# Optimization experiments

Measured on AMD Instinct MI355X. Metric: run time of the kernel, lower is better.

Reference implementation:

```python
import jax, jax.numpy as jnp
import numpy as np

NPG = 128      # nodes per graph = g(4) * e(32), forced by rearrange + cnn1 channels
G, E32 = 4, 32
ALPHA = 1.0    # GCN2Conv(in_channels, 1) -> alpha = 1
BETA = 1.0     # theta=None -> beta = 1


def _gcn_norm(edge_index, edge_weight, n):
    """PyG gcn_norm: add self-loops (w=1), sym-normalize by degree at dst."""
    src, dst = edge_index[0], edge_index[1]
    loop = jnp.arange(n)
    src = jnp.concatenate([src, loop])
    dst = jnp.concatenate([dst, loop])
    w = jnp.concatenate([edge_weight, jnp.ones((n,), edge_weight.dtype)])
    deg = jax.ops.segment_sum(w, dst, num_segments=n)
    dinv = jnp.where(deg > 0, jax.lax.rsqrt(deg), 0.0)
    norm = dinv[src] * w * dinv[dst]
    return src, dst, norm


def _propagate(x, src, dst, norm, n):
    # gather -> weight -> scatter-add (SpMM)
    return jax.ops.segment_sum(x[src] * norm[:, None], dst, num_segments=n)


def setup_inputs() -> dict:
    key = jax.random.key(0)
    ks = jax.random.split(key, 10)
    N, E, C, H, CH = 65536, 524288, 128, 512, 256
    x = jax.random.normal(ks[0], (N, C), jnp.float32)
    edge_index = jax.random.randint(ks[1], (2, E), 0, N, dtype=jnp.int64)
    edge_attr = jax.random.uniform(ks[2], (E,), jnp.float32)
    w1_gcn2 = jax.random.normal(ks[3], (C, C), jnp.float32) / np.float32(np.sqrt(C))
    w_gcn = jax.random.normal(ks[4], (C, H), jnp.float32) / np.float32(np.sqrt(C))
    b_gcn = jnp.zeros((H,), jnp.float32)
    w_cnn1 = jax.random.normal(ks[5], (H, 4 * H), jnp.float32) / np.float32(np.sqrt(4 * H))
    b_cnn1 = jnp.zeros((H,), jnp.float32)
    w_cnn2 = jax.random.normal(ks[6], (CH, H), jnp.float32) / np.float32(np.sqrt(H))
    b_cnn2 = jnp.zeros((CH,), jnp.float32)
    w_lin = jax.random.normal(ks[7], (32 * CH,), jnp.float32) / np.float32(np.sqrt(32 * CH))
    b_lin = jnp.zeros((), jnp.float32)
    return {"x": x, "edge_attr": edge_attr, "w1_gcn2": w1_gcn2, "w_gcn": w_gcn,
            "b_gcn": b_gcn, "w_cnn1": w_cnn1, "b_cnn1": b_cnn1, "w_cnn2": w_cnn2,
            "b_cnn2": b_cnn2, "w_lin": w_lin, "b_lin": b_lin, "edge_index": edge_index}


def reference(x, edge_attr, w1_gcn2, w_gcn, b_gcn, w_cnn1, b_cnn1, w_cnn2, b_cnn2,
              w_lin, b_lin, edge_index):
    n = x.shape[0]
    bs = n // NPG
    src, dst, norm = _gcn_norm(edge_index, edge_attr, n)

    # GCN2Conv(C, layer=1): h = (1-a)*A_hat x + a*x0; out = (1-b)*h + b*(h @ W1)
    h = _propagate(x, src, dst, norm, n)
    h = h * (1.0 - ALPHA) + ALPHA * x
    h = (1.0 - BETA) * h + BETA * (h @ w1_gcn2)

    # GCNConv(C, H): A_hat (h @ W) + b
    h = _propagate(h @ w_gcn, src, dst, norm, n) + b_gcn
    h = jnp.tanh(h)

    f = h.shape[1]  # hidden_channels
    # '(bs g e) f -> bs (g f) e', e=32, g=4
    h = h.reshape(bs, G, E32, f).transpose(0, 1, 3, 2).reshape(bs, G * f, E32)
    # 1x1 convs == per-position linears over channel dim
    h = jax.nn.relu(jnp.einsum('bce,oc->boe', h, w_cnn1) + b_cnn1[None, :, None])
    h = jax.nn.relu(jnp.einsum('bce,oc->boe', h, w_cnn2) + b_cnn2[None, :, None])
    # dropout p=0.5 is identity in eval mode
    h = h.reshape(bs, -1)
    out = h @ w_lin + b_lin
    return jax.nn.sigmoid(out)
```

## Files before the change

### kernel.cpp

```cpp
#include <hip/hip_runtime.h>
#include <hip/hip_bf16.h>

#define N_NODES 65536
#define N_EDGES 524288

typedef __attribute__((ext_vector_type(8))) short bf16x8;
typedef __attribute__((ext_vector_type(4))) float f32x4;

__device__ __forceinline__ float bf2f(unsigned short u) {
    union { unsigned int i; float f; } v;
    v.i = ((unsigned int)u) << 16;
    return v.f;
}
__device__ __forceinline__ unsigned short f2bf(float f) {
    union { float f; unsigned int i; } v;
    v.f = f;
    unsigned int r = v.i + 0x7fff + ((v.i >> 16) & 1);
    return (unsigned short)(r >> 16);
}

__global__ void init_k(int* __restrict__ cnt, float* __restrict__ logits) {
    int i = blockIdx.x * 256 + threadIdx.x;
    cnt[i] = 0;
    if (i < 512) logits[i] = 0.0f;
}
__global__ void cnt_k(const int* __restrict__ dst, int* __restrict__ cnt) {
    int e = blockIdx.x * 256 + threadIdx.x;
    atomicAdd(&cnt[dst[e]], 1);
}

__global__ __launch_bounds__(256) void scan1_k(const int* __restrict__ cnt,
                                               int* __restrict__ rp,
                                               int* __restrict__ bsum) {
    __shared__ int s[256];
    int t = threadIdx.x, g = blockIdx.x * 256 + t;
    int v = cnt[g];
    s[t] = v;
    __syncthreads();
    for (int d = 1; d < 256; d <<= 1) {
        int u = (t >= d) ? s[t - d] : 0;
        __syncthreads();
        s[t] += u;
        __syncthreads();
    }
    rp[g] = s[t] - v;
    if (t == 255) bsum[blockIdx.x] = s[255];
}
__global__ __launch_bounds__(256) void scan2_k(int* __restrict__ bsum,
                                               int* __restrict__ rp) {
    __shared__ int s[256];
    int t = threadIdx.x;
    int v = bsum[t];
    s[t] = v;
    __syncthreads();
    for (int d = 1; d < 256; d <<= 1) {
        int u = (t >= d) ? s[t - d] : 0;
        __syncthreads();
        s[t] += u;
        __syncthreads();
    }
    bsum[t] = s[t] - v;
    if (t == 255) rp[65536] = s[255];
}
__global__ __launch_bounds__(256) void scan3_k(int* __restrict__ rp,
                                               const int* __restrict__ bsum,
                                               int* __restrict__ cursor) {
    int t = threadIdx.x, g = blockIdx.x * 256 + t;
    int r = rp[g] + bsum[blockIdx.x];
    rp[g] = r;
    cursor[g] = r;
}

__global__ void scatter_k(const int* __restrict__ src, const int* __restrict__ dst,
                          const float* __restrict__ w,
                          int* __restrict__ cursor, uint2* __restrict__ ep) {
    int e = blockIdx.x * 256 + threadIdx.x;
    int pos = atomicAdd(&cursor[dst[e]], 1);
    uint2 p;
    p.x = (unsigned int)src[e];
    p.y = __float_as_uint(w[e]);
    ep[pos] = p;
}

__global__ void rowsum_k(const int* __restrict__ rp, const uint2* __restrict__ ep,
                         float* __restrict__ dinv) {
    int n = blockIdx.x * 256 + threadIdx.x;
    int beg = rp[n], end = rp[n + 1];
    float s = 1.0f;
    for (int i = beg; i < end; ++i) s += __uint_as_float(ep[i].y);
    dinv[n] = rsqrtf(s);
}

__global__ void xscale_k(const float* __restrict__ x, const float* __restrict__ dinv,
                         __hip_bfloat16* __restrict__ xbf) {
    int i = (blockIdx.x * 256 + threadIdx.x) * 4;
    float d = dinv[i >> 7];
    float4 v = *(const float4*)(x + i);
    alignas(8) __hip_bfloat16 tmp[4] = {
        __float2bfloat16(d * v.x), __float2bfloat16(d * v.y),
        __float2bfloat16(d * v.z), __float2bfloat16(d * v.w)};
    *(ushort4*)((unsigned short*)xbf + i) = *(const ushort4*)tmp;
}

__global__ void wprep_k(const float* __restrict__ wc1, __hip_bfloat16* __restrict__ wc1pk,
                        const float* __restrict__ wc2, __hip_bfloat16* __restrict__ wc2bf,
                        const float* __restrict__ w1, const float* __restrict__ wg,
                        __hip_bfloat16* __restrict__ WTpk) {
    int bid = blockIdx.x;
    if (bid < 512) {
        int t = bid * 256 + threadIdx.x;
        int l = t & 63, grp = t >> 6;
        int kt = grp & 63, nb = grp >> 6;
        int n = nb * 16 + (l & 15);
        int k0 = kt * 32 + (l >> 4) * 8;
        const float* src = wc1 + (size_t)n * 2048 + k0;
        alignas(16) __hip_bfloat16 tmp[8];
#pragma unroll
        for (int e = 0; e < 8; ++e) tmp[e] = __float2bfloat16(src[e]);
        *(ushort4*)((unsigned short*)wc1pk + (size_t)t * 8)     = *(const ushort4*)tmp;
        *(ushort4*)((unsigned short*)wc1pk + (size_t)t * 8 + 4) = *(const ushort4*)(tmp + 4);
    } else if (bid < 640) {
        int i = (bid - 512) * 1024 + threadIdx.x * 4;
        float4 v = *(const float4*)(wc2 + i);
        alignas(8) __hip_bfloat16 tmp[4] = {__float2bfloat16(v.x), __float2bfloat16(v.y),
                                            __float2bfloat16(v.z), __float2bfloat16(v.w)};
        *(ushort4*)((unsigned short*)wc2bf + i) = *(const ushort4*)tmp;
    } else {
        int t = (bid - 640) * 256 + threadIdx.x;
        int f = t >> 7, c = t & 127;
        float s = 0.f;
#pragma unroll 8
        for (int m = 0; m < 128; ++m) s += w1[c * 128 + m] * wg[m * 512 + f];
        int pk = ((((f >> 4) * 4 + (c >> 5)) * 64 + ((c >> 3) & 3) * 16 + (f & 15)) * 8) + (c & 7);
        WTpk[pk] = __float2bfloat16(s);
    }
}

__global__ __launch_bounds__(256) void gather_k(const int* __restrict__ rp,
                                                const uint2* __restrict__ ep,
                                                const unsigned short* __restrict__ xbf,
                                                const float* __restrict__ dinv,
                                                __hip_bfloat16* __restrict__ ybf) {
    int n = (blockIdx.x * 256 + threadIdx.x) >> 6;
    int lane = threadIdx.x & 63;
    int beg = rp[n], end = rp[n + 1];
    float accx, accy;
    {
        unsigned int u = *(const unsigned int*)(xbf + (size_t)n * 128 + lane * 2);
        accx = bf2f((unsigned short)(u & 0xffff));
        accy = bf2f((unsigned short)(u >> 16));
    }
    int i = beg;
    for (; i + 8 <= end; i += 8) {
        uint2 p[8];
        unsigned int u[8];
#pragma unroll
        for (int k = 0; k < 8; ++k) p[k] = ep[i + k];
#pragma unroll
        for (int k = 0; k < 8; ++k)
            u[k] = *(const unsigned int*)(xbf + (size_t)p[k].x * 128 + lane * 2);
#pragma unroll
        for (int k = 0; k < 8; ++k) {
            float c = __uint_as_float(p[k].y);
            accx += c * bf2f((unsigned short)(u[k] & 0xffff));
            accy += c * bf2f((unsigned short)(u[k] >> 16));
        }
    }
    for (; i + 4 <= end; i += 4) {
        uint2 p[4];
        unsigned int u[4];
#pragma unroll
        for (int k = 0; k < 4; ++k) p[k] = ep[i + k];
#pragma unroll
        for (int k = 0; k < 4; ++k)
            u[k] = *(const unsigned int*)(xbf + (size_t)p[k].x * 128 + lane * 2);
#pragma unroll
        for (int k = 0; k < 4; ++k) {
            float c = __uint_as_float(p[k].y);
            accx += c * bf2f((unsigned short)(u[k] & 0xffff));
            accy += c * bf2f((unsigned short)(u[k] >> 16));
        }
    }
    for (; i < end; ++i) {
        uint2 p = ep[i];
        unsigned int u = *(const unsigned int*)(xbf + (size_t)p.x * 128 + lane * 2);
        float c = __uint_as_float(p.y);
        accx += c * bf2f((unsigned short)(u & 0xffff));
        accy += c * bf2f((unsigned short)(u >> 16));
    }
    float dn = dinv[n];
    accx *= dn;
    accy *= dn;
    alignas(4) __hip_bfloat16 o[2] = {__float2bfloat16(accx), __float2bfloat16(accy)};
    *(unsigned int*)((unsigned short*)ybf + (size_t)n * 128 + lane * 2) =
        *(const unsigned int*)o;
}

__device__ __forceinline__ void gll16(const void* g, void* l) {
    __builtin_amdgcn_global_load_lds(
        (const __attribute__((address_space(1))) void*)g,
        (__attribute__((address_space(3))) void*)l, 16, 0, 0);
}

__global__ __launch_bounds__(512) void fh2c1_k(
    const __hip_bfloat16* __restrict__ ybf,
    const __hip_bfloat16* __restrict__ WTpk,
    const float* __restrict__ bg,
    const __hip_bfloat16* __restrict__ wc1pk,
    const float* __restrict__ bc1,
    __hip_bfloat16* __restrict__ act1) {
    __shared__ char yt[8192];
    __shared__ char ht[16384];
    const int tid = threadIdx.x;
    const int lane = tid & 63, wid = tid >> 6;
    const int bx = blockIdx.x;
    const int l15 = lane & 15, lhi = lane >> 4;

    const __hip_bfloat16* Bp[4];
#pragma unroll
    for (int j = 0; j < 4; ++j)
        Bp[j] = wc1pk + ((size_t)(wid * 4 + j) * 64) * 512 + lane * 8;

    f32x4 acc[2][4] = {};

    for (int g = 0; g < 4; ++g) {
        __syncthreads();
        {
            int r = wid * 4 + (lane >> 4);
            int node = bx * 128 + g * 32 + r;
            int scol = ((lane & 15) ^ (r & 7)) << 4;
            gll16((const char*)ybf + (size_t)node * 256 + scol,
                  yt + wid * 1024 + lane * 16);
        }
        __syncthreads();

        for (int h = 0; h < 2; ++h) {
            f32x4 hacc[2][2];
#pragma unroll
            for (int i = 0; i < 2; ++i)
#pragma unroll
                for (int j = 0; j < 2; ++j) hacc[i][j] = (f32x4){0.f, 0.f, 0.f, 0.f};
#pragma unroll
            for (int kt = 0; kt < 4; ++kt) {
                bf16x8 af[2], bfr[2];
#pragma unroll
                for (int i = 0; i < 2; ++i) {
                    int r = i * 16 + l15;
                    int s = (kt * 4 + lhi) ^ (r & 7);
                    af[i] = *(const bf16x8*)(yt + r * 256 + s * 16);
                }
#pragma unroll
                for (int j = 0; j < 2; ++j) {
                    int nb = h * 16 + wid * 2 + j;
                    bfr[j] = *(const bf16x8*)(WTpk +
                        ((size_t)(nb * 4 + kt) * 64 + lane) * 8);
                }
#pragma unroll
                for (int i = 0; i < 2; ++i)
#pragma unroll
                    for (int j = 0; j < 2; ++j)
                        hacc[i][j] = __builtin_amdgcn_mfma_f32_16x16x32_bf16(
                            bfr[j], af[i], hacc[i][j], 0, 0, 0);
            }
            __syncthreads();
#pragma unroll
            for (int j = 0; j < 2; ++j) {
                int coln = h * 256 + wid * 32 + j * 16 + lhi * 4;
                float4 bgv = *(const float4*)(bg + coln);
                int bytecol = (wid * 32 + j * 16 + lhi * 4) * 2;
                int s = bytecol >> 4;
                int off8 = bytecol & 15;
#pragma unroll
                for (int i = 0; i < 2; ++i) {
                    int row = i * 16 + l15;
                    alignas(8) unsigned short o[4];
#pragma unroll
                    for (int r = 0; r < 4; ++r) {
                        float v = hacc[i][j][r] + ((const float*)&bgv)[r];
                        v = 1.0f - 2.0f / (__expf(2.0f * v) + 1.0f);
                        o[r] = f2bf(v);
                    }
                    *(uint2*)(ht + row * 512 + ((s ^ (row & 7)) << 4) + off8) =
                        *(const uint2*)o;
                }
            }
            __syncthreads();

            const int ktb = g * 16 + h * 8;
            bf16x8 b0[4], b1[4];
#pragma unroll
            for (int j = 0; j < 4; ++j)
                b0[j] = *(const bf16x8*)(Bp[j] + (size_t)ktb * 512);
#pragma unroll
            for (int kk = 0; kk < 8; kk += 2) {
#pragma unroll
                for (int j = 0; j < 4; ++j)
                    b1[j] = *(const bf16x8*)(Bp[j] + (size_t)(ktb + kk + 1) * 512);
                {
                    bf16x8 af[2];
#pragma unroll
                    for (int i = 0; i < 2; ++i) {
                        int r = i * 16 + l15;
                        int s = (kk * 4 + lhi) ^ (r & 7);
                        af[i] = *(const bf16x8*)(ht + r * 512 + s * 16);
                    }
#pragma unroll
                    for (int i = 0; i < 2; ++i)
#pragma unroll
                        for (int j = 0; j < 4; ++j)
                            acc[i][j] = __builtin_amdgcn_mfma_f32_16x16x32_bf16(
                                b0[j], af[i], acc[i][j], 0, 0, 0);
                }
                if (kk + 2 < 8) {
#pragma unroll
                    for (int j = 0; j < 4; ++j)
                        b0[j] = *(const bf16x8*)(Bp[j] + (size_t)(ktb + kk + 2) * 512);
                }
                {
                    bf16x8 af[2];
#pragma unroll
                    for (int i = 0; i < 2; ++i) {
                        int r = i * 16 + l15;
                        int s = ((kk + 1) * 4 + lhi) ^ (r & 7);
                        af[i] = *(const bf16x8*)(ht + r * 512 + s * 16);
                    }
#pragma unroll
                    for (int i = 0; i < 2; ++i)
#pragma unroll
                        for (int j = 0; j < 4; ++j)
                            acc[i][j] = __builtin_amdgcn_mfma_f32_16x16x32_bf16(
                                b1[j], af[i], acc[i][j], 0, 0, 0);
                }
            }
        }
    }

#pragma unroll
    for (int i = 0; i < 2; ++i) {
        int m = bx * 32 + i * 16 + l15;
#pragma unroll
        for (int j = 0; j < 4; ++j) {
            int n = wid * 64 + j * 16 + lhi * 4;
            float4 bv = *(const float4*)(bc1 + n);
            ushort4 o;
#pragma unroll
            for (int r = 0; r < 4; ++r) {
                float v = fmaxf(acc[i][j][r] + ((const float*)&bv)[r], 0.f);
                ((unsigned short*)&o)[r] = f2bf(v);
            }
            *(ushort4*)((unsigned short*)act1 + (size_t)m * 512 + n) = o;
        }
    }
}

template <int ACT, int OUT_MODE, int SWIZ_NTX>
__global__ __launch_bounds__(256) void gemm_mfma_k(
    const __hip_bfloat16* __restrict__ A, const __hip_bfloat16* __restrict__ B,
    const float* __restrict__ bias, void* __restrict__ Cout,
    const float* __restrict__ wlin, int M, int N, int K) {
    __shared__ char lds[65536];

    const int tid = threadIdx.x;
    const int lane = tid & 63, wid = tid >> 6;
    int bx, by;
    if (SWIZ_NTX > 0) {
        int orig = blockIdx.x;
        int per = gridDim.x / (8 * SWIZ_NTX);
        int xcd = orig & 7, k = orig >> 3;
        by = xcd * per + k / SWIZ_NTX;
        bx = k % SWIZ_NTX;
    } else {
        bx = blockIdx.x;
        by = blockIdx.y;
    }
    const int bm = by * 128, bn = bx * 128;
    const int wr = wid >> 1, wc = wid & 1;

    const int srow = wid * 16 + (lane >> 2);
    const int skcol = (((lane & 3) ^ ((lane >> 3) & 3))) * 8;
    const __hip_bfloat16* Abase = A + (size_t)(bm + srow) * K + skcol;
    const __hip_bfloat16* Bbase = B + (size_t)(bn + srow) * K + skcol;
    const int ldso = wid * 1024;

    f32x4 acc[4][4] = {};

    const int lrow = lane & 15;
    const int lkb = (((lane >> 4) ^ ((lane >> 1) & 3)) << 4);
    const int nk = K >> 5;

    auto stage = [&](int buf, int kt) {
        char* la = lds + buf * 16384;
        char* lb = la + 8192;
        gll16(Abase + kt * 32,                  la + ldso);
        gll16(Abase + kt * 32 + (size_t)64 * K, la + 4096 + ldso);
        gll16(Bbase + kt * 32,                  lb + ldso);
        gll16(Bbase + kt * 32 + (size_t)64 * K, lb + 4096 + ldso);
    };

    stage(0, 0);
    stage(1, 1);
    stage(2, 2);

    for (int kt = 0; kt < nk; ++kt) {
        int ahead = nk - 1 - kt;
        if (ahead >= 2)      asm volatile("s_waitcnt vmcnt(8)" ::: "memory");
        else if (ahead == 1) asm volatile("s_waitcnt vmcnt(4)" ::: "memory");
        else                 asm volatile("s_waitcnt vmcnt(0)" ::: "memory");
        __builtin_amdgcn_s_barrier();
        asm volatile("" ::: "memory");
        if (kt + 3 < nk) stage((kt + 3) & 3, kt + 3);

        const char* la = lds + (kt & 3) * 16384;
        const char* lb = la + 8192;
        bf16x8 af[4], bfr[4];
#pragma unroll
        for (int i = 0; i < 4; ++i)
            af[i] = *(const bf16x8*)(la + (wr * 64 + i * 16 + lrow) * 64 + lkb);
#pragma unroll
        for (int j = 0; j < 4; ++j)
            bfr[j] = *(const bf16x8*)(lb + (wc * 64 + j * 16 + lrow) * 64 + lkb);
        __builtin_amdgcn_s_setprio(1);
#pragma unroll
        for (int i = 0; i < 4; ++i)
#pragma unroll
            for (int j = 0; j < 4; ++j)
                acc[i][j] = __builtin_amdgcn_mfma_f32_16x16x32_bf16(
                    bfr[j], af[i], acc[i][j], 0, 0, 0);
        __builtin_amdgcn_s_setprio(0);
        asm volatile("" ::: "memory");
    }

    const int l15 = lane & 15, lhi = lane >> 4;

    if (OUT_MODE == 3) {
        float p0 = 0.f, p1 = 0.f;
#pragma unroll
        for (int i = 0; i < 4; ++i) {
            int e = (i & 1) * 16 + l15;
#pragma unroll
            for (int j = 0; j < 4; ++j) {
                int n = bn + wc * 64 + j * 16 + lhi * 4;
                float4 bv = *(const float4*)(bias + n);
#pragma unroll
                for (int r = 0; r < 4; ++r) {
                    float v = fmaxf(acc[i][j][r] + ((const float*)&bv)[r], 0.f);
                    float wl = wlin[(n + r) * 32 + e];
                    if (i < 2) p0 += v * wl; else p1 += v * wl;
                }
            }
        }
#pragma unroll
        for (int off = 32; off > 0; off >>= 1) {
            p0 += __shfl_down(p0, off, 64);
            p1 += __shfl_down(p1, off, 64);
        }
        if (lane == 0) {
            int g = (bm >> 5) + wr * 2;
            atomicAdd(&((float*)Cout)[g], p0);
            atomicAdd(&((float*)Cout)[g + 1], p1);
        }
        return;
    }

#pragma unroll
    for (int i = 0; i < 4; ++i) {
        int m = bm + wr * 64 + i * 16 + l15;
#pragma unroll
        for (int j = 0; j < 4; ++j) {
            int n = bn + wc * 64 + j * 16 + lhi * 4;
            float4 bv = *(const float4*)(bias + n);
            ushort4 o;
#pragma unroll
            for (int r = 0; r < 4; ++r) {
                float v = acc[i][j][r] + ((const float*)&bv)[r];
                if (ACT == 1) v = fmaxf(v, 0.f);
                ((unsigned short*)&o)[r] = f2bf(v);
            }
            *(ushort4*)((unsigned short*)Cout + (size_t)m * N + n) = o;
        }
    }
}

__global__ void sigmoid_k(const float* __restrict__ logits,
                          const float* __restrict__ blin, float* __restrict__ out) {
    int b = blockIdx.x * 256 + threadIdx.x;
    out[b] = 1.0f / (1.0f + expf(-(logits[b] + blin[0])));
}

extern "C" void kernel_launch(void* const* d_in, const int* in_sizes, int n_in,
                              void* d_out, int out_size, void* d_ws, size_t ws_size,
                              hipStream_t stream) {
    const float* x    = (const float*)d_in[0];
    const float* eattr= (const float*)d_in[1];
    const float* w1   = (const float*)d_in[2];
    const float* wg   = (const float*)d_in[3];
    const float* bg   = (const float*)d_in[4];
    const float* wc1  = (const float*)d_in[5];
    const float* bc1  = (const float*)d_in[6];
    const float* wc2  = (const float*)d_in[7];
    const float* bc2  = (const float*)d_in[8];
    const float* wlin = (const float*)d_in[9];
    const float* blin = (const float*)d_in[10];
    const int*   ei   = (const int*)d_in[11];
    const int* esrc = ei;
    const int* edst = ei + N_EDGES;
    float* out = (float*)d_out;

    char* ws = (char*)d_ws;
    float*          dinv   = (float*)(ws + 0);
    int*            cnt    = (int*)(ws + 262144);
    int*            rp     = (int*)(ws + 524288);
    int*            cursor = (int*)(ws + 786688);
    uint2*          ep     = (uint2*)(ws + 1048832);
    __hip_bfloat16* WTpk   = (__hip_bfloat16*)(ws + 5243136);
    __hip_bfloat16* ybf    = (__hip_bfloat16*)(ws + 5374208);
    __hip_bfloat16* act1   = (__hip_bfloat16*)(ws + 89260288);
    __hip_bfloat16* wc1pk  = (__hip_bfloat16*)(ws + 106037504);
    __hip_bfloat16* wc2bf  = (__hip_bfloat16*)(ws + 108134656);
    __hip_bfloat16* xbf    = (__hip_bfloat16*)(ws + 108396800);
    float*          logits = (float*)(ws + 125174016);
    int*            bsum   = (int*)(ws + 125176064);
    if (ws_size < (size_t)125177088) return;

    init_k<<<N_NODES / 256, 256, 0, stream>>>(cnt, logits);

    cnt_k<<<N_EDGES / 256, 256, 0, stream>>>(edst, cnt);

    scan1_k<<<256, 256, 0, stream>>>(cnt, rp, bsum);
    scan2_k<<<1, 256, 0, stream>>>(bsum, rp);
    scan3_k<<<256, 256, 0, stream>>>(rp, bsum, cursor);

    scatter_k<<<N_EDGES / 256, 256, 0, stream>>>(esrc, edst, eattr, cursor, ep);

    rowsum_k<<<N_NODES / 256, 256, 0, stream>>>(rp, ep, dinv);

    wprep_k<<<896, 256, 0, stream>>>(wc1, wc1pk, wc2, wc2bf, w1, wg, WTpk);
    xscale_k<<<(N_NODES * 128 / 4) / 256, 256, 0, stream>>>(x, dinv, xbf);

    gather_k<<<N_NODES / 4, 256, 0, stream>>>(rp, ep,
                                              (const unsigned short*)xbf, dinv, ybf);

    fh2c1_k<<<512, 512, 0, stream>>>(ybf, WTpk, bg, wc1pk, bc1, act1);

    gemm_mfma_k<1, 3, 0><<<dim3(2, 128), 256, 0, stream>>>(
        act1, wc2bf, bc2, logits, wlin, 16384, 256, 512);

    sigmoid_k<<<2, 256, 0, stream>>>(logits, blin, out);
}
```

Measured before the change: 198.5 us.

## Double-buffer Y tile loads and deepen weight prefetch in fused GCN+conv1 kernel

Doubles the LDS buffer for the per-group Y tile so the next group's async global-to-LDS load is issued during the conv1 MFMA phase of the current group. This removes one barrier and the exposed load latency per group. The conv1 weight fragments now use a 4-deep register prefetch ring instead of 2-deep, which hides more global latency at the cost of more VGPRs and 8KB more LDS per block, and that may reduce occupancy.

New measurement: 195.1 us (median of 2 runs). No clear change (-1.7%).

```diff
diff --git a/kernel.cpp b/kernel.cpp
--- a/kernel.cpp
+++ b/kernel.cpp
@@ -209,7 +209,7 @@
     const __hip_bfloat16* __restrict__ wc1pk,
     const float* __restrict__ bc1,
     __hip_bfloat16* __restrict__ act1) {
-    __shared__ char yt[8192];
+    __shared__ char yt[16384];
     __shared__ char ht[16384];
     const int tid = threadIdx.x;
     const int lane = tid & 63, wid = tid >> 6;
@@ -221,18 +221,22 @@
     for (int j = 0; j < 4; ++j)
         Bp[j] = wc1pk + ((size_t)(wid * 4 + j) * 64) * 512 + lane * 8;
 
+    auto stageY = [&](int buf, int g) {
+        int r = wid * 4 + (lane >> 4);
+        int node = bx * 128 + g * 32 + r;
+        int scol = ((lane & 15) ^ (r & 7)) << 4;
+        gll16((const char*)ybf + (size_t)node * 256 + scol,
+              yt + buf * 8192 + wid * 1024 + lane * 16);
+    };
+
     f32x4 acc[2][4] = {};
 
+    stageY(0, 0);
+    __syncthreads();
+
     for (int g = 0; g < 4; ++g) {
-        __syncthreads();
-        {
-            int r = wid * 4 + (lane >> 4);
-            int node = bx * 128 + g * 32 + r;
-            int scol = ((lane & 15) ^ (r & 7)) << 4;
-            gll16((const char*)ybf + (size_t)node * 256 + scol,
-                  yt + wid * 1024 + lane * 16);
-        }
-        __syncthreads();
+        if (g > 0) __syncthreads();
+        const char* ytc = yt + (g & 1) * 8192;
 
         for (int h = 0; h < 2; ++h) {
             f32x4 hacc[2][2];
@@ -247,7 +251,7 @@
                 for (int i = 0; i < 2; ++i) {
                     int r = i * 16 + l15;
                     int s = (kt * 4 + lhi) ^ (r & 7);
-                    af[i] = *(const bf16x8*)(yt + r * 256 + s * 16);
+                    af[i] = *(const bf16x8*)(ytc + r * 256 + s * 16);
                 }
 #pragma unroll
                 for (int j = 0; j < 2; ++j) {
@@ -286,50 +290,35 @@
             }
             __syncthreads();
 
+            if (h == 1 && g < 3) stageY((g + 1) & 1, g + 1);
+
             const int ktb = g * 16 + h * 8;
-            bf16x8 b0[4], b1[4];
-#pragma unroll
-            for (int j = 0; j < 4; ++j)
-                b0[j] = *(const bf16x8*)(Bp[j] + (size_t)ktb * 512);
-#pragma unroll
-            for (int kk = 0; kk < 8; kk += 2) {
+            bf16x8 bb[4][4];
+#pragma unroll
+            for (int d = 0; d < 4; ++d)
 #pragma unroll
                 for (int j = 0; j < 4; ++j)
-                    b1[j] = *(const bf16x8*)(Bp[j] + (size_t)(ktb + kk + 1) * 512);
-                {
-                    bf16x8 af[2];
-#pragma unroll
-                    for (int i = 0; i < 2; ++i) {
-                        int r = i * 16 + l15;
-                        int s = (kk * 4 + lhi) ^ (r & 7);
-                        af[i] = *(const bf16x8*)(ht + r * 512 + s * 16);
-                    }
-#pragma unroll
-                    for (int i = 0; i < 2; ++i)
-#pragma unroll
-                        for (int j = 0; j < 4; ++j)
-                            acc[i][j] = __builtin_amdgcn_mfma_f32_16x16x32_bf16(
-                                b0[j], af[i], acc[i][j], 0, 0, 0);
+                    bb[d][j] = *(const bf16x8*)(Bp[j] + (size_t)(ktb + d) * 512);
+#pragma unroll
+            for (int kk = 0; kk < 8; ++kk) {
+                bf16x8 af[2];
+#pragma unroll
+                for (int i = 0; i < 2; ++i) {
+                    int r = i * 16 + l15;
+                    int s = (kk * 4 + lhi) ^ (r & 7);
+                    af[i] = *(const bf16x8*)(ht + r * 512 + s * 16);
                 }
-                if (kk + 2 < 8) {
+#pragma unroll
+                for (int i = 0; i < 2; ++i)
 #pragma unroll
                     for (int j = 0; j < 4; ++j)
-                        b0[j] = *(const bf16x8*)(Bp[j] + (size_t)(ktb + kk + 2) * 512);
-                }
-                {
-                    bf16x8 af[2];
-#pragma unroll
-                    for (int i = 0; i < 2; ++i) {
-                        int r = i * 16 + l15;
-                        int s = ((kk + 1) * 4 + lhi) ^ (r & 7);
-                        af[i] = *(const bf16x8*)(ht + r * 512 + s * 16);
-                    }
-#pragma unroll
-                    for (int i = 0; i < 2; ++i)
-#pragma unroll
-                        for (int j = 0; j < 4; ++j)
-                            acc[i][j] = __builtin_amdgcn_mfma_f32_16x16x32_bf16(
-                                b1[j], af[i], acc[i][j], 0, 0, 0);
+                        acc[i][j] = __builtin_amdgcn_mfma_f32_16x16x32_bf16(
+                            bb[kk & 3][j], af[i], acc[i][j], 0, 0, 0);
+                if (kk + 4 < 8) {
+#pragma unroll
+                    for (int j = 0; j < 4; ++j)
+                        bb[kk & 3][j] =
+                            *(const bf16x8*)(Bp[j] + (size_t)(ktb + kk + 4) * 512);
                 }
             }
         }
```
